# Optimization experiments

Hardware: AMD Instinct MI355X
Metric: run time of the kernel (lower is better)

The kernel has to match this reference:

```python
import math
import jax, jax.numpy as jnp
import numpy as np

D_MODEL = 1024
N_HEAD = 16
D_HEAD = 64
Q_LEN = 2048
MEM_LEN = 2048
K_LEN = MEM_LEN + Q_LEN
B = 1
LN_EPS = 1e-5


def setup_inputs() -> dict:
    key = jax.random.key(0)
    ks = jax.random.split(key, 8)
    hidden = jax.random.normal(ks[0], (B, Q_LEN, D_MODEL), dtype=jnp.float32)
    position_embedding = jax.random.normal(ks[1], (K_LEN, D_MODEL), dtype=jnp.float32)
    u = jax.random.normal(ks[2], (N_HEAD, D_HEAD), dtype=jnp.float32) * 0.02
    v = jax.random.normal(ks[3], (N_HEAD, D_HEAD), dtype=jnp.float32) * 0.02
    memory = jax.random.normal(ks[4], (B, MEM_LEN, D_MODEL), dtype=jnp.float32)
    # TXL causal mask: query i may attend to key j iff j <= i + MEM_LEN
    i = jnp.arange(Q_LEN)[:, None]
    j = jnp.arange(K_LEN)[None, :]
    mask = (j > (i + MEM_LEN))[None, None]  # (1,1,Q,K) bool, True = masked
    # weights (torch Linear has no bias here); stored as (in, out)
    s = 1.0 / math.sqrt(D_MODEL)
    W_qkv = jax.random.normal(ks[5], (D_MODEL, 3 * N_HEAD * D_HEAD), dtype=jnp.float32) * s
    W_pe = jax.random.normal(ks[6], (D_MODEL, N_HEAD * D_HEAD), dtype=jnp.float32) * s
    W_out = jax.random.normal(ks[7], (N_HEAD * D_HEAD, D_MODEL), dtype=jnp.float32) * (1.0 / math.sqrt(N_HEAD * D_HEAD))
    return {"hidden": hidden, "position_embedding": position_embedding, "u": u,
            "v": v, "mask": mask, "memory": memory,
            "W_qkv": W_qkv, "W_pe": W_pe, "W_out": W_out}


def _layer_norm(x):
    # elementwise_affine=False LayerNorm over last dim
    mu = jnp.mean(x, axis=-1, keepdims=True)
    var = jnp.var(x, axis=-1, keepdims=True)
    return (x - mu) / jnp.sqrt(var + LN_EPS)


def reference(hidden, position_embedding, u, v, mask, memory, W_qkv, W_pe, W_out):
    batch, q_len, _ = hidden.shape
    k_len = position_embedding.shape[0]
    scale = 1.0 / math.sqrt(D_HEAD)

    mh = jnp.concatenate([memory, hidden], axis=1)          # (B, k_len, d_model)
    qkv = mh @ W_qkv                                        # post-norm: no LN on input
    Q, K, V = jnp.split(qkv, 3, axis=-1)
    Q = Q[:, -q_len:, :]
    pe = position_embedding @ W_pe                          # (k_len, H*D)

    Q = Q.reshape(batch, q_len, N_HEAD, D_HEAD)
    K = K.reshape(batch, k_len, N_HEAD, D_HEAD)
    V = V.reshape(batch, k_len, N_HEAD, D_HEAD)
    pe = pe.reshape(batch, k_len, N_HEAD, D_HEAD)

    AC = jnp.einsum('bqhd,bkhd->bhqk', Q + u, K)
    BD = jnp.einsum('bqhd,bkhd->bhqk', Q + v, pe)
    # NOTE: the original module calls relative_shift(BD) but DISCARDS the
    # result, so BD is used unshifted. We faithfully reproduce that.
    score = (AC + BD) * scale
    score = jnp.where(mask, -jnp.inf, score)
    prob = jax.nn.softmax(score, axis=-1)                   # (B,H,Q,K)
    av = jnp.einsum('bhqk,bkhd->bqhd', prob, V)
    av = av.reshape(batch, q_len, N_HEAD * D_HEAD)
    attn_out = av @ W_out
    return _layer_norm(hidden + attn_out)                   # post-norm residual
```

## Files before the change

### kernel.cpp

```cpp
#include <hip/hip_runtime.h>

typedef __attribute__((ext_vector_type(4))) float f32x4;
typedef __attribute__((ext_vector_type(16))) float f32x16;
typedef __attribute__((ext_vector_type(8))) short bf16x8;
typedef __attribute__((ext_vector_type(4))) unsigned short u16x4;
typedef unsigned short u16;

#define DM 1024
#define NHEAD 16
#define DHEAD 64
#define QLEN 2048
#define MLEN 2048
#define KLEN 4096

__device__ __forceinline__ float bf2f(u16 u) {
    unsigned i = ((unsigned)u) << 16; float f; __builtin_memcpy(&f, &i, 4); return f;
}
__device__ __forceinline__ u16 f2bf(float f) {
    unsigned i; __builtin_memcpy(&i, &f, 4);
    unsigned r = i + 0x7fffu + ((i >> 16) & 1u);
    return (u16)(r >> 16);
}
__device__ __forceinline__ unsigned cvtpk_bf16(float lo, float hi) {
    unsigned r;
    asm("v_cvt_pk_bf16_f32 %0, %1, %2" : "=v"(r) : "v"(lo), "v"(hi));
    return r;
}
__device__ __forceinline__ void gl2lds16(const void* g, void* l) {
    __builtin_amdgcn_global_load_lds((const __attribute__((address_space(1))) void*)g,
                                     (__attribute__((address_space(3))) void*)l, 16, 0, 0);
}

__global__ __launch_bounds__(256) void prep(
    const float* __restrict__ memory, const float* __restrict__ hidden,
    const float* __restrict__ pos, const float* __restrict__ Wqkv,
    const float* __restrict__ Wpe, const float* __restrict__ Wout,
    u16* __restrict__ MH, u16* __restrict__ PEA,
    u16* __restrict__ WQKVT, u16* __restrict__ WPET, u16* __restrict__ WOUTT)
{
    __shared__ float ls[64][65];
    const int b = blockIdx.x, t = threadIdx.x;
    if (b < 8192) {
        size_t e = ((size_t)b * 256 + t) * 4;
        const size_t HALF = (size_t)KLEN * DM;
        f32x4 v; u16* dst;
        if (e < HALF) {
            size_t row = e >> 10, col = e & 1023;
            const float* src = (row < MLEN) ? (memory + row * DM) : (hidden + (row - MLEN) * DM);
            v = *(const f32x4*)(src + col);
            dst = MH + e;
        } else {
            size_t e2 = e - HALF;
            v = *(const f32x4*)(pos + e2);
            dst = PEA + e2;
        }
        u16x4 o;
        #pragma unroll
        for (int c = 0; c < 4; ++c) o[c] = f2bf(v[c]);
        *(u16x4*)dst = o;
        return;
    }
    int tb = b - 8192;
    const float* src; u16* dst; int N, bx, by;
    if (tb < 768)       { src = Wqkv; dst = WQKVT; N = 3 * DM; bx = tb % 48; by = tb / 48; }
    else if (tb < 1024) { int i = tb - 768;  src = Wpe;  dst = WPET;  N = DM; bx = i & 15; by = i >> 4; }
    else                { int i = tb - 1024; src = Wout; dst = WOUTT; N = DM; bx = i & 15; by = i >> 4; }
    const int n0 = bx * 64, k0 = by * 64;
    const int c = t & 63, rg = t >> 6;
    #pragma unroll
    for (int p = 0; p < 16; ++p) {
        int r = p * 4 + rg;
        ls[r][c] = src[(size_t)(k0 + r) * N + n0 + c];
    }
    __syncthreads();
    #pragma unroll
    for (int p = 0; p < 16; ++p) {
        int r = p * 4 + rg;
        dst[(size_t)(n0 + r) * DM + k0 + c] = f2bf(ls[c][r]);
    }
}

__global__ __launch_bounds__(256, 2) void gemm_qkvpe(
    const u16* __restrict__ MH, const u16* __restrict__ PEA,
    const u16* __restrict__ WQKVT, const u16* __restrict__ WPET,
    const float* __restrict__ u, const float* __restrict__ vv,
    u16* __restrict__ QHAT, u16* __restrict__ KHAT, u16* __restrict__ VB)
{
    __shared__ u16 lsA[128 * 64];
    __shared__ u16 lsB[128 * 64];
    const int b = blockIdx.x;
    int row0, col0, region; const u16 *A, *B;
    if (b < 512)      { row0 = (b >> 4) * 128; col0 = 1024 + (b & 15) * 128; A = MH; B = WQKVT;
                        region = (col0 < 2048) ? 1 : 2; }
    else if (b < 640) { int i = b - 512; row0 = 2048 + (i >> 3) * 128; col0 = (i & 7) * 128;
                        A = MH; B = WQKVT; region = 0; }
    else              { int i = b - 640; row0 = (i >> 3) * 128; col0 = (i & 7) * 128;
                        A = PEA; B = WPET; region = 3; }
    const int tid = threadIdx.x, wave = tid >> 6, lane = tid & 63;
    const int blk = lane >> 4, ln = lane & 15;
    const int wr = (wave >> 1) << 6, wc = (wave & 1) << 6;
    const int rstage = lane >> 3;
    const int cstage = (lane & 7) * 8;

    f32x4 acc[4][4];
    #pragma unroll
    for (int i = 0; i < 4; ++i)
        #pragma unroll
        for (int j = 0; j < 4; ++j) acc[i][j] = f32x4{0.f, 0.f, 0.f, 0.f};

    for (int k0 = 0; k0 < DM; k0 += 64) {
        #pragma unroll
        for (int t = 0; t < 4; ++t) {
            int chunk = wave * 4 + t;
            int r = chunk * 8 + rstage;
            gl2lds16(A + (size_t)(row0 + r) * DM + k0 + cstage, lsA + chunk * 512);
            gl2lds16(B + (size_t)(col0 + r) * DM + k0 + cstage, lsB + chunk * 512);
        }
        __syncthreads();
        #pragma unroll
        for (int kk = 0; kk < 2; ++kk) {
            bf16x8 af[4], bfr[4];
            #pragma unroll
            for (int i = 0; i < 4; ++i)
                af[i] = *(const bf16x8*)(lsA + (wr + i * 16 + ln) * 64 + kk * 32 + blk * 8);
            #pragma unroll
            for (int j = 0; j < 4; ++j)
                bfr[j] = *(const bf16x8*)(lsB + (wc + j * 16 + ln) * 64 + kk * 32 + blk * 8);
            #pragma unroll
            for (int i = 0; i < 4; ++i)
                #pragma unroll
                for (int j = 0; j < 4; ++j)
                    acc[i][j] = __builtin_amdgcn_mfma_f32_16x16x32_bf16(af[i], bfr[j], acc[i][j], 0, 0, 0);
        }
        __syncthreads();
    }
    #pragma unroll
    for (int i = 0; i < 4; ++i)
        #pragma unroll
        for (int j = 0; j < 4; ++j)
            #pragma unroll
            for (int r = 0; r < 4; ++r) {
                int row = row0 + wr + i * 16 + blk * 4 + r;
                int col = col0 + wc + j * 16 + ln;
                float val = acc[i][j][r];
                if (region == 0) {
                    int q = row - MLEN, h = col >> 6;
                    size_t base = ((size_t)h * QLEN + q) * 128 + (col & 63);
                    QHAT[base]      = f2bf((val + u[col]) * 0.125f);
                    QHAT[base + 64] = f2bf((val + vv[col]) * 0.125f);
                } else if (region == 1) {
                    int c = col - 1024, h = c >> 6;
                    KHAT[((size_t)h * KLEN + row) * 128 + (c & 63)] = f2bf(val);
                } else if (region == 2) {
                    VB[(size_t)row * DM + (col - 2048)] = f2bf(val);
                } else {
                    int h = col >> 6;
                    KHAT[((size_t)h * KLEN + row) * 128 + 64 + (col & 63)] = f2bf(val);
                }
            }
}

__global__ __launch_bounds__(256) void pack_vt(const u16* __restrict__ VB, u16* __restrict__ VT)
{
    __shared__ float ls[64][65];
    const int kt = blockIdx.x, h = blockIdx.y;
    const int t = threadIdx.x, c = t & 63, rg = t >> 6;
    #pragma unroll
    for (int p = 0; p < 16; ++p) {
        int r = p * 4 + rg;
        ls[r][c] = bf2f(VB[(size_t)(kt * 64 + r) * DM + h * 64 + c]);
    }
    __syncthreads();
    #pragma unroll
    for (int p = 0; p < 16; ++p) {
        int d = p * 4 + rg;
        VT[((size_t)h * DHEAD + d) * KLEN + kt * 64 + c] = f2bf(ls[c][d]);
    }
}

__global__ __launch_bounds__(256, 4) void attn_fused(
    const u16* __restrict__ QHAT, const u16* __restrict__ KHAT,
    const u16* __restrict__ VT, u16* __restrict__ OPb, float* __restrict__ ML)
{
    __shared__ __align__(16) u16 smem[17408];
    const int b = blockIdx.x;
    const int h  = ((b & 7) << 1) | ((b >> 3) & 1);
    const int qb = (b >> 4) & 15;
    const int ks = b >> 8;
    const int tid = threadIdx.x;
    const int wave = tid >> 6, lane = tid & 63;
    const int l31 = lane & 31, hi = lane >> 5;
    const int qrow0 = qb * 128 + wave * 32;
    u16* pb = smem + 12288 + wave * 1280;
    const int px = (l31 >> 3) & 3;

    const u16* khp = KHAT + (size_t)h * KLEN * 128;
    const u16* vhp = VT + (size_t)h * DHEAD * KLEN;

    const int nt = qb + 17;
    const int kbase = ks * nt * 32;

    auto stage = [&](int buf, int kt) {
        const int k0 = kbase + kt * 32;
        u16* Kb = smem + buf * 4096;
        u16* Vb = smem + 8192 + buf * 2048;
        #pragma unroll
        for (int i = 0; i < 2; ++i) {
            int c = i * 256 + tid;
            int row = c >> 4, cgl = c & 15;
            int cs = cgl ^ (row & 15);
            gl2lds16(khp + ((size_t)(k0 + row) << 7) + cs * 8,
                     Kb + (size_t)(i * 256 + (tid & ~63)) * 8);
        }
        {
            int row = tid >> 2, cgl = tid & 3;
            int cs = cgl ^ (row & 3);
            gl2lds16(vhp + (size_t)row * KLEN + k0 + cs * 8,
                     Vb + (size_t)(tid & ~63) * 8);
        }
    };

    bf16x8 qf[8];
    {
        const u16* qbase = QHAT + ((size_t)h * QLEN + qrow0 + l31) * 128 + hi * 8;
        #pragma unroll
        for (int kd = 0; kd < 8; ++kd) qf[kd] = *(const bf16x8*)(qbase + kd * 16);
    }

    f32x16 oacc[2];
    #pragma unroll
    for (int dg = 0; dg < 2; ++dg)
        #pragma unroll
        for (int r = 0; r < 16; ++r) oacc[dg][r] = 0.f;
    float mi = -1e30f, li = 0.f;

    const int qlim = qrow0 + 31 + MLEN;
    const int qsel = qrow0 + l31 + MLEN;

    stage(0, 0);
    asm volatile("s_waitcnt vmcnt(0)" ::: "memory");
    __syncthreads();

    int cur = 0;
    for (int kt = 0; kt < nt; ++kt) {
        const int k0 = kbase + kt * 32;
        if (kt + 1 < nt) stage(cur ^ 1, kt + 1);

        if (k0 <= qlim) {
            f32x16 sacc;
            #pragma unroll
            for (int r = 0; r < 16; ++r) sacc[r] = 0.f;
            const u16* kb = smem + cur * 4096;
            const int rx = l31 & 15;
            #pragma unroll
            for (int kd = 0; kd < 8; ++kd) {
                int cd = (kd * 2 + hi) ^ rx;
                bf16x8 kf = *(const bf16x8*)(kb + l31 * 128 + cd * 8);
                sacc = __builtin_amdgcn_mfma_f32_32x32x16_bf16(kf, qf[kd], sacc, 0, 0, 0);
            }
            if (k0 + 31 > qrow0 + MLEN) {
                const int keyb = k0 + 4 * hi;
                #pragma unroll
                for (int r = 0; r < 16; ++r) {
                    int key = keyb + (r & 3) + 8 * (r >> 2);
                    if (key > qsel) sacc[r] = -1e30f;
                }
            }
            float mt = sacc[0];
            #pragma unroll
            for (int r = 1; r < 16; ++r) mt = fmaxf(mt, sacc[r]);
            mt = fmaxf(mt, __shfl_xor(mt, 32, 64));
            if (!__all(mt <= mi)) {
                float mn = fmaxf(mi, mt);
                float corr = __expf(mi - mn);
                mi = mn;
                li *= corr;
                #pragma unroll
                for (int dg = 0; dg < 2; ++dg)
                    #pragma unroll
                    for (int r = 0; r < 16; ++r) oacc[dg][r] *= corr;
            }
            #pragma unroll
            for (int r = 0; r < 16; ++r) sacc[r] = __expf(sacc[r] - mi);
            float rs = sacc[0];
            #pragma unroll
            for (int r = 1; r < 16; ++r) rs += sacc[r];
            li += rs + __shfl_xor(rs, 32, 64);
            {
                unsigned* pd = (unsigned*)(pb + (size_t)l31 * 40);
                #pragma unroll
                for (int b2 = 0; b2 < 4; ++b2)
                    #pragma unroll
                    for (int c = 0; c < 2; ++c)
                        pd[(b2 ^ px) * 4 + 2 * hi + c] =
                            cvtpk_bf16(sacc[4 * b2 + 2 * c], sacc[4 * b2 + 2 * c + 1]);
            }
            #pragma unroll
            for (int kkl = 0; kkl < 2; ++kkl) {
                bf16x8 pf = *(const bf16x8*)(pb + (size_t)l31 * 40 + ((kkl * 2 + hi) ^ px) * 8);
                #pragma unroll
                for (int dg = 0; dg < 2; ++dg) {
                    int vrow = dg * 32 + l31;
                    int cd = (kkl * 2 + hi) ^ (vrow & 3);
                    bf16x8 vf = *(const bf16x8*)(smem + 8192 + cur * 2048 + vrow * 32 + cd * 8);
                    oacc[dg] = __builtin_amdgcn_mfma_f32_32x32x16_bf16(vf, pf, oacc[dg], 0, 0, 0);
                }
            }
        }
        asm volatile("s_waitcnt vmcnt(0)" ::: "memory");
        __syncthreads();
        cur ^= 1;
    }

    const int q = qrow0 + l31;
    unsigned* op32 = (unsigned*)(OPb + (((size_t)ks * QLEN + q) * NHEAD + h) * 64);
    #pragma unroll
    for (int dg = 0; dg < 2; ++dg) {
        union { f32x16 v; float f[16]; } oo;
        oo.v = oacc[dg];
        #pragma unroll
        for (int b2 = 0; b2 < 4; ++b2)
            #pragma unroll
            for (int c = 0; c < 2; ++c)
                op32[(dg * 32 + 8 * b2 + 4 * hi) / 2 + c] =
                    cvtpk_bf16(oo.f[4 * b2 + 2 * c], oo.f[4 * b2 + 2 * c + 1]);
    }
    if (!hi) {
        float* ml = ML + (((size_t)ks * QLEN + q) * NHEAD + h) * 2;
        ml[0] = mi; ml[1] = li;
    }
}

__global__ __launch_bounds__(256) void attn_combine(
    const u16* __restrict__ OPb, const float* __restrict__ ML, u16* __restrict__ AVB)
{
    int idx = blockIdx.x * 256 + threadIdx.x;
    int d8 = (idx & 7) * 8;
    int h  = (idx >> 3) & 15;
    int q  = idx >> 7;
    float m[4], l[4], mf = -1e30f;
    #pragma unroll
    for (int ks = 0; ks < 4; ++ks) {
        const float* ml = ML + (((size_t)ks * QLEN + q) * NHEAD + h) * 2;
        m[ks] = ml[0]; l[ks] = ml[1];
        mf = fmaxf(mf, m[ks]);
    }
    float lsum = 0.f;
    float a[4];
    #pragma unroll
    for (int ks = 0; ks < 4; ++ks) {
        a[ks] = __expf(m[ks] - mf);
        lsum += a[ks] * l[ks];
    }
    float inv = 1.f / lsum;
    float acc[8];
    #pragma unroll
    for (int j = 0; j < 8; ++j) acc[j] = 0.f;
    #pragma unroll
    for (int ks = 0; ks < 4; ++ks) {
        float w = a[ks] * inv;
        const u16* src = OPb + (((size_t)ks * QLEN + q) * NHEAD + h) * 64 + d8;
        u16x4 x0 = *(const u16x4*)(src);
        u16x4 x1 = *(const u16x4*)(src + 4);
        #pragma unroll
        for (int j = 0; j < 4; ++j) { acc[j] += w * bf2f(x0[j]); acc[4 + j] += w * bf2f(x1[j]); }
    }
    unsigned* A32 = (unsigned*)AVB;
    size_t base = ((size_t)q * DM + h * 64 + d8) >> 1;
    #pragma unroll
    for (int j = 0; j < 4; ++j)
        A32[base + j] = cvtpk_bf16(acc[2 * j], acc[2 * j + 1]);
}

__global__ __launch_bounds__(256, 2) void gemm_out(
    const u16* __restrict__ A, const u16* __restrict__ Bt, float* __restrict__ RES)
{
    __shared__ u16 lsA[128 * 64];
    __shared__ u16 lsB[128 * 64];
    const int b = blockIdx.x;
    const int tile = b >> 1, kh = b & 1;
    const int row0 = (tile >> 3) * 128, col0 = (tile & 7) * 128;
    const int tid = threadIdx.x, wave = tid >> 6, lane = tid & 63;
    const int blk = lane >> 4, ln = lane & 15;
    const int wr = (wave >> 1) << 6, wc = (wave & 1) << 6;
    const int rstage = lane >> 3;
    const int cstage = (lane & 7) * 8;

    f32x4 acc[4][4];
    #pragma unroll
    for (int i = 0; i < 4; ++i)
        #pragma unroll
        for (int j = 0; j < 4; ++j) acc[i][j] = f32x4{0.f, 0.f, 0.f, 0.f};

    for (int k0 = kh * 512; k0 < kh * 512 + 512; k0 += 64) {
        #pragma unroll
        for (int t = 0; t < 4; ++t) {
            int chunk = wave * 4 + t;
            int r = chunk * 8 + rstage;
            gl2lds16(A  + (size_t)(row0 + r) * DM + k0 + cstage, lsA + chunk * 512);
            gl2lds16(Bt + (size_t)(col0 + r) * DM + k0 + cstage, lsB + chunk * 512);
        }
        __syncthreads();
        #pragma unroll
        for (int kk = 0; kk < 2; ++kk) {
            bf16x8 af[4], bfr[4];
            #pragma unroll
            for (int i = 0; i < 4; ++i)
                af[i] = *(const bf16x8*)(lsA + (wr + i * 16 + ln) * 64 + kk * 32 + blk * 8);
            #pragma unroll
            for (int j = 0; j < 4; ++j)
                bfr[j] = *(const bf16x8*)(lsB + (wc + j * 16 + ln) * 64 + kk * 32 + blk * 8);
            #pragma unroll
            for (int i = 0; i < 4; ++i)
                #pragma unroll
                for (int j = 0; j < 4; ++j)
                    acc[i][j] = __builtin_amdgcn_mfma_f32_16x16x32_bf16(af[i], bfr[j], acc[i][j], 0, 0, 0);
        }
        __syncthreads();
    }
    float* C = RES + (size_t)kh * QLEN * DM;
    #pragma unroll
    for (int i = 0; i < 4; ++i)
        #pragma unroll
        for (int j = 0; j < 4; ++j)
            #pragma unroll
            for (int r = 0; r < 4; ++r) {
                int row = row0 + wr + i * 16 + blk * 4 + r;
                int col = col0 + wc + j * 16 + ln;
                C[(size_t)row * DM + col] = acc[i][j][r];
            }
}

__global__ __launch_bounds__(256) void ln_kernel(
    const float* __restrict__ hidden, const float* __restrict__ RES, float* __restrict__ out)
{
    const int row = blockIdx.x, t = threadIdx.x;
    const int wave = t >> 6, lane = t & 63;
    __shared__ float ws[8];
    f32x4 a = ((const f32x4*)(hidden + (size_t)row * DM))[t];
    f32x4 r0 = ((const f32x4*)(RES + (size_t)row * DM))[t];
    f32x4 r1 = ((const f32x4*)(RES + (size_t)(QLEN + row) * DM))[t];
    f32x4 v;
    #pragma unroll
    for (int c = 0; c < 4; ++c) v[c] = a[c] + r0[c] + r1[c];
    float s = v[0] + v[1] + v[2] + v[3];
    float s2 = v[0] * v[0] + v[1] * v[1] + v[2] * v[2] + v[3] * v[3];
    #pragma unroll
    for (int off = 1; off < 64; off <<= 1) {
        s += __shfl_xor(s, off, 64);
        s2 += __shfl_xor(s2, off, 64);
    }
    if (lane == 0) { ws[wave] = s; ws[4 + wave] = s2; }
    __syncthreads();
    float ts = ws[0] + ws[1] + ws[2] + ws[3];
    float ts2 = ws[4] + ws[5] + ws[6] + ws[7];
    float mu = ts * (1.f / DM);
    float var = ts2 * (1.f / DM) - mu * mu;
    float rsq = rsqrtf(var + 1e-5f);
    f32x4 o;
    #pragma unroll
    for (int c = 0; c < 4; ++c) o[c] = (v[c] - mu) * rsq;
    ((f32x4*)(out + (size_t)row * DM))[t] = o;
}

extern "C" void kernel_launch(void* const* d_in, const int* in_sizes, int n_in,
                              void* d_out, int out_size, void* d_ws, size_t ws_size,
                              hipStream_t stream)
{
    const float* hidden = (const float*)d_in[0];
    const float* pos    = (const float*)d_in[1];
    const float* u      = (const float*)d_in[2];
    const float* vv     = (const float*)d_in[3];
    const float* memory = (const float*)d_in[5];
    const float* Wqkv   = (const float*)d_in[6];
    const float* Wpe    = (const float*)d_in[7];
    const float* Wout   = (const float*)d_in[8];
    float* out = (float*)d_out;

    char* w = (char*)d_ws;
    auto alloc = [&](size_t bytes) {
        void* p = (void*)w;
        w += (bytes + 255) & ~(size_t)255;
        return p;
    };
    u16* MH    = (u16*)alloc((size_t)KLEN * DM * 2);
    u16* PEA   = (u16*)alloc((size_t)KLEN * DM * 2);
    u16* WQKVT = (u16*)alloc((size_t)3 * DM * DM * 2);
    u16* WPET  = (u16*)alloc((size_t)DM * DM * 2);
    u16* VB    = (u16*)alloc((size_t)KLEN * DM * 2);
    u16* QHAT  = (u16*)alloc((size_t)NHEAD * QLEN * 128 * 2);
    u16* KHAT  = (u16*)alloc((size_t)NHEAD * KLEN * 128 * 2);
    u16* VTb   = (u16*)alloc((size_t)NHEAD * DHEAD * KLEN * 2);
    u16* AVB   = (u16*)alloc((size_t)QLEN * DM * 2);
    float* RES = (float*)alloc((size_t)2 * QLEN * DM * 4);
    u16* WOUTT = (u16*)alloc((size_t)DM * DM * 2);
    u16* OPb   = (u16*)d_ws;
    float* ML  = (float*)((char*)d_ws + (size_t)4 * QLEN * NHEAD * 64 * 2);

    prep<<<8192 + 1280, 256, 0, stream>>>(memory, hidden, pos, Wqkv, Wpe, Wout,
                                          MH, PEA, WQKVT, WPET, WOUTT);
    gemm_qkvpe<<<896, 256, 0, stream>>>(MH, PEA, WQKVT, WPET, u, vv, QHAT, KHAT, VB);
    pack_vt<<<dim3(KLEN / 64, NHEAD), 256, 0, stream>>>(VB, VTb);
    attn_fused<<<dim3(1024), 256, 0, stream>>>(QHAT, KHAT, VTb, OPb, ML);
    attn_combine<<<dim3(QLEN * NHEAD * 8 / 256), 256, 0, stream>>>(OPb, ML, AVB);
    gemm_out<<<256, 256, 0, stream>>>(AVB, WOUTT, RES);
    ln_kernel<<<QLEN, 256, 0, stream>>>(hidden, RES, out);
}
```

Baseline: 171.0 us.

## Stage V through registers with padded LDS, rotate q-block order, raise occupancy

```diff
diff --git a/kernel.cpp b/kernel.cpp
--- a/kernel.cpp
+++ b/kernel.cpp
@@ -80,7 +80,7 @@
     }
 }
 
-__global__ __launch_bounds__(256, 2) void gemm_qkvpe(
+__global__ __launch_bounds__(256, 3) void gemm_qkvpe(
     const u16* __restrict__ MH, const u16* __restrict__ PEA,
     const u16* __restrict__ WQKVT, const u16* __restrict__ WPET,
     const float* __restrict__ u, const float* __restrict__ vv,
@@ -182,16 +182,16 @@
     const u16* __restrict__ QHAT, const u16* __restrict__ KHAT,
     const u16* __restrict__ VT, u16* __restrict__ OPb, float* __restrict__ ML)
 {
-    __shared__ __align__(16) u16 smem[17408];
+    __shared__ __align__(16) u16 smem[18432];
     const int b = blockIdx.x;
     const int h  = ((b & 7) << 1) | ((b >> 3) & 1);
-    const int qb = (b >> 4) & 15;
     const int ks = b >> 8;
+    const int qb = (((b >> 4) & 15) + 4 * ks) & 15;
     const int tid = threadIdx.x;
     const int wave = tid >> 6, lane = tid & 63;
     const int l31 = lane & 31, hi = lane >> 5;
     const int qrow0 = qb * 128 + wave * 32;
-    u16* pb = smem + 12288 + wave * 1280;
+    u16* pb = smem + 13312 + wave * 1280;
     const int px = (l31 >> 3) & 3;
 
     const u16* khp = KHAT + (size_t)h * KLEN * 128;
@@ -199,11 +199,12 @@
 
     const int nt = qb + 17;
     const int kbase = ks * nt * 32;
-
-    auto stage = [&](int buf, int kt) {
+    const int vd = tid >> 2, vc = tid & 3;
+    const int vslot = vc ^ ((vd >> 3) & 3);
+
+    auto stage_load = [&](int buf, int kt) -> bf16x8 {
         const int k0 = kbase + kt * 32;
         u16* Kb = smem + buf * 4096;
-        u16* Vb = smem + 8192 + buf * 2048;
         #pragma unroll
         for (int i = 0; i < 2; ++i) {
             int c = i * 256 + tid;
@@ -212,12 +213,10 @@
             gl2lds16(khp + ((size_t)(k0 + row) << 7) + cs * 8,
                      Kb + (size_t)(i * 256 + (tid & ~63)) * 8);
         }
-        {
-            int row = tid >> 2, cgl = tid & 3;
-            int cs = cgl ^ (row & 3);
-            gl2lds16(vhp + (size_t)row * KLEN + k0 + cs * 8,
-                     Vb + (size_t)(tid & ~63) * 8);
-        }
+        return *(const bf16x8*)(vhp + (size_t)vd * KLEN + k0 + vc * 8);
+    };
+    auto stage_write = [&](int buf, bf16x8 vr) {
+        *(bf16x8*)(smem + 8192 + buf * 2560 + vd * 40 + vslot * 8) = vr;
     };
 
     bf16x8 qf[8];
@@ -237,14 +236,16 @@
     const int qlim = qrow0 + 31 + MLEN;
     const int qsel = qrow0 + l31 + MLEN;
 
-    stage(0, 0);
+    bf16x8 vreg = stage_load(0, 0);
     asm volatile("s_waitcnt vmcnt(0)" ::: "memory");
+    stage_write(0, vreg);
     __syncthreads();
 
     int cur = 0;
     for (int kt = 0; kt < nt; ++kt) {
         const int k0 = kbase + kt * 32;
-        if (kt + 1 < nt) stage(cur ^ 1, kt + 1);
+        const bool pre = (kt + 1 < nt);
+        if (pre) vreg = stage_load(cur ^ 1, kt + 1);
 
         if (k0 <= qlim) {
             f32x16 sacc;
@@ -266,9 +267,14 @@
                     if (key > qsel) sacc[r] = -1e30f;
                 }
             }
-            float mt = sacc[0];
-            #pragma unroll
-            for (int r = 1; r < 16; ++r) mt = fmaxf(mt, sacc[r]);
+            float mt;
+            {
+                f32x4 m4;
+                #pragma unroll
+                for (int r = 0; r < 4; ++r)
+                    m4[r] = fmaxf(fmaxf(sacc[r], sacc[4 + r]), fmaxf(sacc[8 + r], sacc[12 + r]));
+                mt = fmaxf(fmaxf(m4[0], m4[1]), fmaxf(m4[2], m4[3]));
+            }
             mt = fmaxf(mt, __shfl_xor(mt, 32, 64));
             if (!__all(mt <= mi)) {
                 float mn = fmaxf(mi, mt);
@@ -282,9 +288,14 @@
             }
             #pragma unroll
             for (int r = 0; r < 16; ++r) sacc[r] = __expf(sacc[r] - mi);
-            float rs = sacc[0];
-            #pragma unroll
-            for (int r = 1; r < 16; ++r) rs += sacc[r];
+            float rs;
+            {
+                f32x4 s4;
+                #pragma unroll
+                for (int r = 0; r < 4; ++r)
+                    s4[r] = (sacc[r] + sacc[4 + r]) + (sacc[8 + r] + sacc[12 + r]);
+                rs = (s4[0] + s4[1]) + (s4[2] + s4[3]);
+            }
             li += rs + __shfl_xor(rs, 32, 64);
             {
                 unsigned* pd = (unsigned*)(pb + (size_t)l31 * 40);
@@ -301,13 +312,14 @@
                 #pragma unroll
                 for (int dg = 0; dg < 2; ++dg) {
                     int vrow = dg * 32 + l31;
-                    int cd = (kkl * 2 + hi) ^ (vrow & 3);
-                    bf16x8 vf = *(const bf16x8*)(smem + 8192 + cur * 2048 + vrow * 32 + cd * 8);
+                    int cd = (kkl * 2 + hi) ^ ((l31 >> 3) & 3);
+                    bf16x8 vf = *(const bf16x8*)(smem + 8192 + cur * 2560 + vrow * 40 + cd * 8);
                     oacc[dg] = __builtin_amdgcn_mfma_f32_32x32x16_bf16(vf, pf, oacc[dg], 0, 0, 0);
                 }
             }
         }
         asm volatile("s_waitcnt vmcnt(0)" ::: "memory");
+        if (pre) stage_write(cur ^ 1, vreg);
         __syncthreads();
         cur ^= 1;
     }
@@ -372,7 +384,7 @@
         A32[base + j] = cvtpk_bf16(acc[2 * j], acc[2 * j + 1]);
 }
 
-__global__ __launch_bounds__(256, 2) void gemm_out(
+__global__ __launch_bounds__(256, 3) void gemm_out(
     const u16* __restrict__ A, const u16* __restrict__ Bt, float* __restrict__ RES)
 {
     __shared__ u16 lsA[128 * 64];
```

New measurement: 163.4 us. 4.4% less time.
